# Performance work log

Measured on AMD Instinct MI355X. Metric: run time of the kernel, lower is better.

Reference implementation:

```python
import jax, jax.numpy as jnp
import numpy as np

GROUP_SIZE = 64  # matches init_kwargs group_size


def setup_inputs() -> dict:
    key = jax.random.key(0)
    k1, k2, k3, k4 = jax.random.split(key, 4)
    B, S, D_in, D_out = 4, 2048, 4096, 4096
    x = jax.random.normal(k1, (B, S, D_in), dtype=jnp.float32)
    # symmetric int8 quantized weights in [-127, 127]
    weight_quant = jax.random.randint(k2, (D_out, D_in), -127, 128, dtype=jnp.int32)
    num_groups = (D_out * D_in) // GROUP_SIZE
    # positive per-group scales (abs_max / 127 of a typical weight group)
    weight_scale = jax.random.uniform(k3, (num_groups,), dtype=jnp.float32,
                                      minval=1e-3, maxval=2e-2)
    bias = jax.random.normal(k4, (D_out,), dtype=jnp.float32) * 0.01
    return {"x": x, "weight_quant": weight_quant,
            "weight_scale": weight_scale, "bias": bias}


def reference(x, weight_quant, weight_scale, bias):
    # Group-wise symmetric dequantization: flatten row-major, scale each
    # contiguous group of GROUP_SIZE elements by its own scale.
    out_f, in_f = weight_quant.shape
    w = weight_quant.astype(jnp.float32).reshape(-1, GROUP_SIZE)  # [num_groups, G]
    w = w * weight_scale[:, None]
    w = w.reshape(out_f, in_f).astype(x.dtype)
    # F.linear(x, W, b) = x @ W^T + b
    return jnp.einsum('bsi,oi->bso', x, w) + bias
```

## Files before the change

### kernel.cpp

```cpp
#include <hip/hip_runtime.h>
#include <stdint.h>


typedef __attribute__((ext_vector_type(8))) short short8;
typedef __attribute__((ext_vector_type(8))) unsigned short ushort8;
typedef __attribute__((ext_vector_type(4))) float f32x4;
typedef __attribute__((ext_vector_type(16))) float f32x16;
typedef __attribute__((ext_vector_type(4))) float float4v;
typedef __attribute__((ext_vector_type(4))) int int4v;

typedef __attribute__((address_space(1))) void g_void;
typedef __attribute__((address_space(3))) void l_void;

__device__ __forceinline__ unsigned short f2bf(float f) {
  union { float f; unsigned int u; } v; v.f = f;
  unsigned int r = v.u + 0x7FFFu + ((v.u >> 16) & 1u);
  return (unsigned short)(r >> 16);
}

__device__ __forceinline__ void async_copy16(const void* g, void* l) {
  __builtin_amdgcn_global_load_lds((const g_void*)g, (l_void*)l, 16, 0, 0);
}

__device__ __forceinline__ void wg_barrier() {
  asm volatile("" ::: "memory");
  __builtin_amdgcn_s_barrier();
  asm volatile("" ::: "memory");
}

#define WAIT_VMCNT(N) asm volatile("s_waitcnt vmcnt(" #N ")" ::: "memory")

__global__ __launch_bounds__(256) void cvt_kernel(
    const float* __restrict__ x, const int* __restrict__ w,
    const float* __restrict__ s, unsigned short* __restrict__ ox,
    unsigned short* __restrict__ ow, int n8x, int n8w, int gx) {
  if ((int)blockIdx.x < gx) {
    const int stride = gx * 256;
    for (int t = blockIdx.x * 256 + threadIdx.x; t < n8x; t += stride) {
      const float4v* xp = (const float4v*)x + (size_t)t * 2;
      float4v a = xp[0], b = xp[1];
      ushort8 r;
      r[0] = f2bf(a[0]); r[1] = f2bf(a[1]); r[2] = f2bf(a[2]); r[3] = f2bf(a[3]);
      r[4] = f2bf(b[0]); r[5] = f2bf(b[1]); r[6] = f2bf(b[2]); r[7] = f2bf(b[3]);
      *(ushort8*)(ox + (size_t)t * 8) = r;
    }
  } else {
    const int stride = ((int)gridDim.x - gx) * 256;
    for (int t = ((int)blockIdx.x - gx) * 256 + threadIdx.x; t < n8w; t += stride) {
      const int4v* wp = (const int4v*)w + (size_t)t * 2;
      int4v q0 = wp[0], q1 = wp[1];
      float sc = s[t >> 3];
      ushort8 r;
      r[0] = f2bf((float)q0[0] * sc); r[1] = f2bf((float)q0[1] * sc);
      r[2] = f2bf((float)q0[2] * sc); r[3] = f2bf((float)q0[3] * sc);
      r[4] = f2bf((float)q1[0] * sc); r[5] = f2bf((float)q1[1] * sc);
      r[6] = f2bf((float)q1[2] * sc); r[7] = f2bf((float)q1[3] * sc);
      *(ushort8*)(ow + (size_t)t * 8) = r;
    }
  }
}


#define MF32(a, b, c) __builtin_amdgcn_mfma_f32_32x32x16_bf16(a, b, c, 0, 0, 0)

#define READ12(AU, BU) do {                              \
    const unsigned char* _a = (AU) + abase;              \
    const unsigned char* _b = (BU) + bbase;              \
    a00 = *(const short8*)(_a + ca0);                    \
    a10 = *(const short8*)(_a + 2048 + ca0);             \
    a20 = *(const short8*)(_a + 4096 + ca0);             \
    a30 = *(const short8*)(_a + 6144 + ca0);             \
    a01 = *(const short8*)(_a + ca1);                    \
    a11 = *(const short8*)(_a + 2048 + ca1);             \
    a21 = *(const short8*)(_a + 4096 + ca1);             \
    a31 = *(const short8*)(_a + 6144 + ca1);             \
    b00 = *(const short8*)(_b + ca0);                    \
    b10 = *(const short8*)(_b + 2048 + ca0);             \
    b01 = *(const short8*)(_b + ca1);                    \
    b11 = *(const short8*)(_b + 2048 + ca1);             \
  } while (0)

#define MFMA16() do {                                    \
    acc[0][0] = MF32(a00, b00, acc[0][0]);               \
    acc[1][0] = MF32(a10, b00, acc[1][0]);               \
    acc[2][0] = MF32(a20, b00, acc[2][0]);               \
    acc[3][0] = MF32(a30, b00, acc[3][0]);               \
    acc[0][1] = MF32(a00, b10, acc[0][1]);               \
    acc[1][1] = MF32(a10, b10, acc[1][1]);               \
    acc[2][1] = MF32(a20, b10, acc[2][1]);               \
    acc[3][1] = MF32(a30, b10, acc[3][1]);               \
    acc[0][0] = MF32(a01, b01, acc[0][0]);               \
    acc[1][0] = MF32(a11, b01, acc[1][0]);               \
    acc[2][0] = MF32(a21, b01, acc[2][0]);               \
    acc[3][0] = MF32(a31, b01, acc[3][0]);               \
    acc[0][1] = MF32(a01, b11, acc[0][1]);               \
    acc[1][1] = MF32(a11, b11, acc[1][1]);               \
    acc[2][1] = MF32(a21, b11, acc[2][1]);               \
    acc[3][1] = MF32(a31, b11, acc[3][1]);               \
  } while (0)

#define PRIO1 __builtin_amdgcn_s_setprio(1)
#define PRIO0 __builtin_amdgcn_s_setprio(0)

__device__ __forceinline__ void stage2(const unsigned short* src, int rstride,
                                       unsigned char* dst) {
  async_copy16(src, dst);
  async_copy16(src + rstride, dst + 8192);
}

__global__ __launch_bounds__(512, 2) void gemm_8p(
    const unsigned short* __restrict__ Xb,
    const unsigned short* __restrict__ Wb,
    const float* __restrict__ bias,
    float* __restrict__ C, int M, int N, int K) {
  __shared__ __align__(16) unsigned char smem[131072];
  const int tid = threadIdx.x;
  const int lane = tid & 63, w = tid >> 6;
  const int wm = w >> 2, wn = w & 3;
  const int l31 = lane & 31, kg = lane >> 5;

  const int nbn = N >> 8;
  int bid = blockIdx.x;
  {
    const int nwg = gridDim.x;
    if ((nwg & 7) == 0) bid = (bid & 7) * (nwg >> 3) + (bid >> 3);
  }
  const int m0 = (bid / nbn) << 8;
  const int n0 = (bid % nbn) << 8;

  const int xr = (l31 >> 1) & 3;
  const int ca0 = ((0 + kg) ^ xr) << 4;
  const int ca1 = ((2 + kg) ^ xr) << 4;
  const int abase = (wm * 128 + l31) * 64;
  const int bbase = (wn * 64 + l31) * 64;

  const int rl = tid >> 2;
  const int lc = (tid & 3) ^ ((tid >> 3) & 3);
  const unsigned short* pA = Xb + (size_t)(m0 + rl) * K + lc * 8;
  const unsigned short* pB = Wb + (size_t)(n0 + rl) * K + lc * 8;
  const int rstride = K << 7;
  const int wuo = w << 10;

  f32x16 acc[4][2];
#pragma unroll
  for (int i = 0; i < 4; i++)
#pragma unroll
    for (int j = 0; j < 2; j++) acc[i][j] = (f32x16)(0.f);

  const int NT = K >> 6;

  stage2(pA, rstride, smem + wuo);
  stage2(pB, rstride, smem + 65536 + wuo);
  stage2(pA + 32, rstride, smem + 16384 + wuo);
  stage2(pB + 32, rstride, smem + 65536 + 16384 + wuo);
  WAIT_VMCNT(4);
  wg_barrier();

  short8 a00, a10, a20, a30, a01, a11, a21, a31, b00, b10, b01, b11;

  for (int t = 0; t < NT - 1; ++t) {
    const int p = t & 1;
    const unsigned char* Au = smem + p * 32768;
    const unsigned char* Bu = smem + 65536 + p * 32768;
    unsigned char* Aq = smem + (p ^ 1) * 32768 + wuo;
    unsigned char* Bq = smem + 65536 + (p ^ 1) * 32768 + wuo;
    const unsigned short* sA = pA + (size_t)(t + 1) * 64;
    const unsigned short* sB = pB + (size_t)(t + 1) * 64;

    READ12(Au, Bu);
    stage2(sA, rstride, Aq);
    stage2(sB, rstride, Bq);
    stage2(sA + 32, rstride, Aq + 16384);
    stage2(sB + 32, rstride, Bq + 16384);
    wg_barrier();
    PRIO1; MFMA16(); PRIO0;
    WAIT_VMCNT(8);
    wg_barrier();
    READ12(Au + 16384, Bu + 16384);
    wg_barrier();
    PRIO1; MFMA16(); PRIO0;
    WAIT_VMCNT(4);
    wg_barrier();
  }

  {
    const int p = (NT - 1) & 1;
    const unsigned char* Au = smem + p * 32768;
    const unsigned char* Bu = smem + 65536 + p * 32768;
    READ12(Au, Bu);
    wg_barrier();
    PRIO1; MFMA16(); PRIO0;
    WAIT_VMCNT(0);
    wg_barrier();
    READ12(Au + 16384, Bu + 16384);
    wg_barrier();
    PRIO1; MFMA16(); PRIO0;
  }

  const int gm = m0 + wm * 128 + 4 * kg;
  const int gn = n0 + wn * 64 + l31;
  const float bv0 = bias[gn], bv1 = bias[gn + 32];
#pragma unroll
  for (int mt = 0; mt < 4; ++mt) {
#pragma unroll
    for (int nt = 0; nt < 2; ++nt) {
      const float bv = nt ? bv1 : bv0;
      const int col = gn + nt * 32;
      f32x16 v = acc[mt][nt];
#pragma unroll
      for (int r = 0; r < 16; ++r) {
        const int row = gm + mt * 32 + (r & 3) + 8 * (r >> 2);
        C[(size_t)row * N + col] = v[r] + bv;
      }
    }
  }
}

#define BM 128
#define BN 128
#define BK 64

__global__ __launch_bounds__(256) void gemm_fused(
    const float* __restrict__ Xf, const int* __restrict__ Wq,
    const float* __restrict__ Ws, const float* __restrict__ bias,
    float* __restrict__ C, int M, int N, int K) {
  __shared__ unsigned char smem[(BM * BK + BN * BK) * 2];
  const int tid = threadIdx.x;
  const int lane = tid & 63, wid = tid >> 6;
  const int m0 = blockIdx.y * BM, n0 = blockIdx.x * BN;
  const int sr = lane >> 3, fc = (lane & 7) ^ sr;
  const int arow = m0 + wid * 32 + sr, brow = n0 + wid * 32 + sr;
  unsigned char* As = smem;
  unsigned char* Bs = smem + BM * BK * 2;
  unsigned char* stA = As + wid * 4096 + lane * 16;
  unsigned char* stB = Bs + wid * 4096 + lane * 16;
  const int l31 = lane & 31, lh = lane >> 5, le = lane & 7;
  const int wm = (wid & 1) * 64, wn = (wid >> 1) * 64;
  const unsigned char* Aw = As + (wm + l31) * 128;
  const unsigned char* Bw = Bs + (wn + l31) * 128;
  const int Kg = K >> 6;

  f32x16 acc[2][2];
#pragma unroll
  for (int i = 0; i < 2; i++)
#pragma unroll
    for (int j = 0; j < 2; j++) acc[i][j] = (f32x16)(0.f);

  for (int k0 = 0; k0 < K; k0 += BK) {
#pragma unroll
    for (int t = 0; t < 4; t++) {
      const float4v* xa = (const float4v*)(Xf + (size_t)(arow + t * 8) * K + k0 + fc * 8);
      float4v x0 = xa[0], x1 = xa[1];
      ushort8 ra;
      ra[0] = f2bf(x0[0]); ra[1] = f2bf(x0[1]); ra[2] = f2bf(x0[2]); ra[3] = f2bf(x0[3]);
      ra[4] = f2bf(x1[0]); ra[5] = f2bf(x1[1]); ra[6] = f2bf(x1[2]); ra[7] = f2bf(x1[3]);
      *(ushort8*)(stA + t * 1024) = ra;
      const int4v* wq = (const int4v*)(Wq + (size_t)(brow + t * 8) * K + k0 + fc * 8);
      int4v q0 = wq[0], q1 = wq[1];
      float sc = Ws[(size_t)(brow + t * 8) * Kg + (k0 >> 6)];
      ushort8 rb;
      rb[0] = f2bf((float)q0[0] * sc); rb[1] = f2bf((float)q0[1] * sc);
      rb[2] = f2bf((float)q0[2] * sc); rb[3] = f2bf((float)q0[3] * sc);
      rb[4] = f2bf((float)q1[0] * sc); rb[5] = f2bf((float)q1[1] * sc);
      rb[6] = f2bf((float)q1[2] * sc); rb[7] = f2bf((float)q1[3] * sc);
      *(ushort8*)(stB + t * 1024) = rb;
    }
    __syncthreads();
#pragma unroll
    for (int s = 0; s < 4; s++) {
      const int off = ((s + 4 * lh) ^ le) << 4;
      short8 a0 = *(const short8*)(Aw + off);
      short8 a1 = *(const short8*)(Aw + 4096 + off);
      short8 b0 = *(const short8*)(Bw + off);
      short8 b1 = *(const short8*)(Bw + 4096 + off);
      acc[0][0] = __builtin_amdgcn_mfma_f32_32x32x16_bf16(a0, b0, acc[0][0], 0, 0, 0);
      acc[0][1] = __builtin_amdgcn_mfma_f32_32x32x16_bf16(a0, b1, acc[0][1], 0, 0, 0);
      acc[1][0] = __builtin_amdgcn_mfma_f32_32x32x16_bf16(a1, b0, acc[1][0], 0, 0, 0);
      acc[1][1] = __builtin_amdgcn_mfma_f32_32x32x16_bf16(a1, b1, acc[1][1], 0, 0, 0);
    }
    __syncthreads();
  }

  const int gm = m0 + wm + 4 * lh, gn = n0 + wn + l31;
#pragma unroll
  for (int j = 0; j < 2; j++) {
    const int col = gn + j * 32;
    const float bv = bias[col];
#pragma unroll
    for (int i = 0; i < 2; i++) {
      const int rbase = gm + i * 32;
      f32x16 v = acc[i][j];
#pragma unroll
      for (int r = 0; r < 16; r++) {
        const int row = rbase + (r & 3) + 8 * (r >> 2);
        C[(size_t)row * N + col] = v[r] + bv;
      }
    }
  }
}

extern "C" void kernel_launch(void* const* d_in, const int* in_sizes, int n_in,
                              void* d_out, int out_size, void* d_ws, size_t ws_size,
                              hipStream_t stream) {
  const float* x = (const float*)d_in[0];
  const int* wq = (const int*)d_in[1];
  const float* wsc = (const float*)d_in[2];
  const float* bias = (const float*)d_in[3];
  float* out = (float*)d_out;

  const int N = in_sizes[3];
  const int K = in_sizes[1] / N;
  const int M = in_sizes[0] / K;

  const size_t needX = (size_t)M * K * 2;
  const size_t needW = (size_t)N * K * 2;
  const bool big = (M % 256 == 0) && (N % 256 == 0) && (K % 64 == 0) && (K >= 128);

  if (big && ws_size >= needX + needW) {
    unsigned short* Xb = (unsigned short*)d_ws;
    unsigned short* Wb = (unsigned short*)((char*)d_ws + needX);
    const int n8x = (M * K) / 8, n8w = (N * K) / 8;
    const int gx = 1376, gw = 688;
    cvt_kernel<<<gx + gw, 256, 0, stream>>>(x, wq, wsc, Xb, Wb, n8x, n8w, gx);
    dim3 grid((M / 256) * (N / 256));
    gemm_8p<<<grid, 512, 0, stream>>>(Xb, Wb, bias, out, M, N, K);
  } else {
    dim3 grid(N / BN, M / BM), block(256);
    gemm_fused<<<grid, block, 0, stream>>>(x, wq, wsc, bias, out, M, N, K);
  }
}
```

Before: 579.8 us.

## Restructure LDS tile layout into k-half units and split async staging across phases

Changes the shared-memory layout so each 32-wide k half of a tile is stored as its own unit with 32-byte rows and a new XOR swizzle, and the fragment reads are remapped to match. Global-to-LDS staging is split so the first half of the next tile is issued before the first MFMA block and the second half before the second, and two barriers per iteration are dropped. The intent is to cut barrier overhead and spread memory traffic more evenly over the compute. The risk is that the reduced synchronisation or the new swizzle causes LDS bank conflicts or read/write races.

After: 571.7 us. No clear change (-1.4%).

```diff
diff --git a/kernel.cpp b/kernel.cpp
--- a/kernel.cpp
+++ b/kernel.cpp
@@ -66,18 +66,18 @@
 #define READ12(AU, BU) do {                              \
     const unsigned char* _a = (AU) + abase;              \
     const unsigned char* _b = (BU) + bbase;              \
-    a00 = *(const short8*)(_a + ca0);                    \
-    a10 = *(const short8*)(_a + 2048 + ca0);             \
-    a20 = *(const short8*)(_a + 4096 + ca0);             \
-    a30 = *(const short8*)(_a + 6144 + ca0);             \
-    a01 = *(const short8*)(_a + ca1);                    \
-    a11 = *(const short8*)(_a + 2048 + ca1);             \
-    a21 = *(const short8*)(_a + 4096 + ca1);             \
-    a31 = *(const short8*)(_a + 6144 + ca1);             \
-    b00 = *(const short8*)(_b + ca0);                    \
-    b10 = *(const short8*)(_b + 2048 + ca0);             \
-    b01 = *(const short8*)(_b + ca1);                    \
-    b11 = *(const short8*)(_b + 2048 + ca1);             \
+    a00 = *(const short8*)(_a + cak);                    \
+    a10 = *(const short8*)(_a + 1024 + cak);             \
+    a20 = *(const short8*)(_a + 2048 + cak);             \
+    a30 = *(const short8*)(_a + 3072 + cak);             \
+    a01 = *(const short8*)(_a + 8192 + cak);             \
+    a11 = *(const short8*)(_a + 8192 + 1024 + cak);      \
+    a21 = *(const short8*)(_a + 8192 + 2048 + cak);      \
+    a31 = *(const short8*)(_a + 8192 + 3072 + cak);      \
+    b00 = *(const short8*)(_b + cak);                    \
+    b10 = *(const short8*)(_b + 1024 + cak);             \
+    b01 = *(const short8*)(_b + 8192 + cak);             \
+    b11 = *(const short8*)(_b + 8192 + 1024 + cak);      \
   } while (0)
 
 #define MFMA16() do {                                    \
@@ -102,10 +102,10 @@
 #define PRIO1 __builtin_amdgcn_s_setprio(1)
 #define PRIO0 __builtin_amdgcn_s_setprio(0)
 
-__device__ __forceinline__ void stage2(const unsigned short* src, int rstride,
-                                       unsigned char* dst) {
-  async_copy16(src, dst);
-  async_copy16(src + rstride, dst + 8192);
+__device__ __forceinline__ void stage_unit(const unsigned short* src,
+                                           unsigned char* dst_unit) {
+  async_copy16(src, dst_unit);
+  async_copy16(src + 16, dst_unit + 8192);
 }
 
 __global__ __launch_bounds__(512, 2) void gemm_8p(
@@ -128,17 +128,14 @@
   const int m0 = (bid / nbn) << 8;
   const int n0 = (bid % nbn) << 8;
 
-  const int xr = (l31 >> 1) & 3;
-  const int ca0 = ((0 + kg) ^ xr) << 4;
-  const int ca1 = ((2 + kg) ^ xr) << 4;
-  const int abase = (wm * 128 + l31) * 64;
-  const int bbase = (wn * 64 + l31) * 64;
-
-  const int rl = tid >> 2;
-  const int lc = (tid & 3) ^ ((tid >> 3) & 3);
-  const unsigned short* pA = Xb + (size_t)(m0 + rl) * K + lc * 8;
-  const unsigned short* pB = Wb + (size_t)(n0 + rl) * K + lc * 8;
-  const int rstride = K << 7;
+  const int cak = ((kg ^ ((l31 >> 2) & 1)) << 4);
+  const int abase = (wm * 128 + l31) * 32;
+  const int bbase = (wn * 64 + l31) * 32;
+
+  const int rowi = tid >> 1;
+  const int kgi = ((tid & 1) ^ ((tid >> 3) & 1)) << 3;
+  const unsigned short* pA = Xb + (size_t)(m0 + rowi) * K + kgi;
+  const unsigned short* pB = Wb + (size_t)(n0 + rowi) * K + kgi;
   const int wuo = w << 10;
 
   f32x16 acc[4][2];
@@ -149,10 +146,10 @@
 
   const int NT = K >> 6;
 
-  stage2(pA, rstride, smem + wuo);
-  stage2(pB, rstride, smem + 65536 + wuo);
-  stage2(pA + 32, rstride, smem + 16384 + wuo);
-  stage2(pB + 32, rstride, smem + 65536 + 16384 + wuo);
+  stage_unit(pA, smem + wuo);
+  stage_unit(pB, smem + 65536 + wuo);
+  stage_unit(pA + 32, smem + 16384 + wuo);
+  stage_unit(pB + 32, smem + 65536 + 16384 + wuo);
   WAIT_VMCNT(4);
   wg_barrier();
 
@@ -168,16 +165,14 @@
     const unsigned short* sB = pB + (size_t)(t + 1) * 64;
 
     READ12(Au, Bu);
-    stage2(sA, rstride, Aq);
-    stage2(sB, rstride, Bq);
-    stage2(sA + 32, rstride, Aq + 16384);
-    stage2(sB + 32, rstride, Bq + 16384);
-    wg_barrier();
+    stage_unit(sA, Aq);
+    stage_unit(sB, Bq);
     PRIO1; MFMA16(); PRIO0;
-    WAIT_VMCNT(8);
+    WAIT_VMCNT(4);
     wg_barrier();
     READ12(Au + 16384, Bu + 16384);
-    wg_barrier();
+    stage_unit(sA + 32, Aq + 16384);
+    stage_unit(sB + 32, Bq + 16384);
     PRIO1; MFMA16(); PRIO0;
     WAIT_VMCNT(4);
     wg_barrier();
@@ -188,12 +183,10 @@
     const unsigned char* Au = smem + p * 32768;
     const unsigned char* Bu = smem + 65536 + p * 32768;
     READ12(Au, Bu);
-    wg_barrier();
     PRIO1; MFMA16(); PRIO0;
     WAIT_VMCNT(0);
     wg_barrier();
     READ12(Au + 16384, Bu + 16384);
-    wg_barrier();
     PRIO1; MFMA16(); PRIO0;
   }
 
```
